# Performance work log

Hardware: AMD Instinct MI355X
Metric: run time of the kernel (lower is better)

## Reference

```python
import jax, jax.numpy as jnp
import numpy as np

EPS = 1e-8  # torch CosineSimilarity default eps

B, T, D, K = 16, 1024, 2048, 64


def setup_inputs() -> dict:
    key = jax.random.key(0)
    k1, k2, k3 = jax.random.split(key, 3)
    inputs = jax.random.normal(k1, (B, T, D), dtype=jnp.float32)
    class_avgs = jax.random.normal(k2, (K, D), dtype=jnp.float32)
    labels = jax.random.randint(k3, (B, T), 0, K, dtype=jnp.int64)
    return {"inputs": inputs, "class_avgs": class_avgs, "labels": labels}


def _simrel_forward(inputs, class_avgs, labels):
    # inputs: [B, T, D]; class_avgs: [K, D]; labels: [B, T] int
    # Faithful training-mode forward: sequential running-mean prototype
    # update per token (row-major over batch then sequence), cosine sims
    # computed against the prototype state *before* each token's update.
    b, t, d = inputs.shape
    k = class_avgs.shape[0]
    vecs = inputs.reshape(b * t, d)
    labs = labels.reshape(b * t)
    class_ids = jnp.arange(k)

    def step(carry, xs):
        avgs, counts = carry          # [K, D], [K]
        vec, label = xs               # [D], scalar int
        nv = jnp.maximum(jnp.sqrt(jnp.sum(vec * vec)), EPS)
        na = jnp.maximum(jnp.sqrt(jnp.sum(avgs * avgs, axis=1)), EPS)  # [K]
        cos = (avgs @ vec) / (na * nv)                                 # [K]
        is_inf = jnp.any(jnp.isinf(avgs), axis=1)                      # [K]
        self_sim = jnp.sum(vec * vec) / (nv * nv)  # cosine(vec, vec)
        is_label = class_ids == label
        sims = jnp.where(is_inf, jnp.where(is_label, self_sim, -1.0), cos)
        # running-mean update of the labeled class prototype
        c = counts[label]
        old = avgs[label]
        new_row = jnp.where(is_inf[label], vec, (old * c + vec) / (c + 1.0))
        avgs = avgs.at[label].set(new_row)
        counts = counts.at[label].add(1.0)
        return (avgs, counts), sims

    counts0 = jnp.zeros((k,), dtype=inputs.dtype)
    (_, _), sims = jax.lax.scan(step, (class_avgs, counts0), (vecs, labs))
    return sims.reshape(b, t, k)


def reference(inputs, class_avgs, labels):
    return _simrel_forward(inputs, class_avgs, labels)
```

## Files before the change

### kernel.cpp

```cpp
#include <hip/hip_runtime.h>
#include <hip/hip_bf16.h>

#define N_TOK 16384
#define DIM 2048
#define KCLS 64
#define JRANGES 32
#define RANGE 512
#define KC 64
#define EPS 1e-8f

typedef short bf16x8 __attribute__((ext_vector_type(8)));
typedef unsigned short u16x8 __attribute__((ext_vector_type(8)));
typedef float f32x4 __attribute__((ext_vector_type(4)));

__device__ __forceinline__ unsigned short f2bf(float f) {
    unsigned u = __float_as_uint(f);
    u += 0x7fffu + ((u >> 16) & 1u);
    return (unsigned short)(u >> 16);
}
__device__ __forceinline__ float bf2f(unsigned short s) {
    return __uint_as_float(((unsigned)s) << 16);
}

__device__ __forceinline__ float dpp_sum64(float x) {
    x += __int_as_float(__builtin_amdgcn_update_dpp(0, __float_as_int(x), 0x111, 0xf, 0xf, true));
    x += __int_as_float(__builtin_amdgcn_update_dpp(0, __float_as_int(x), 0x112, 0xf, 0xf, true));
    x += __int_as_float(__builtin_amdgcn_update_dpp(0, __float_as_int(x), 0x114, 0xf, 0xf, true));
    x += __int_as_float(__builtin_amdgcn_update_dpp(0, __float_as_int(x), 0x118, 0xf, 0xf, true));
    x += __int_as_float(__builtin_amdgcn_update_dpp(0, __float_as_int(x), 0x142, 0xf, 0xf, true));
    x += __int_as_float(__builtin_amdgcn_update_dpp(0, __float_as_int(x), 0x143, 0xf, 0xf, true));
    return x;
}

__global__ __launch_bounds__(256) void prep_kernel(
    const float* __restrict__ x, unsigned short* __restrict__ xb,
    float* __restrict__ vnorm2, const int* __restrict__ raw,
    int* __restrict__ lab, float* __restrict__ n2snap) {
    int bid = blockIdx.x, tid = threadIdx.x;
    if (bid < 64) {
        __shared__ int not64;
        if (tid == 0) not64 = 0;
        __syncthreads();
        int n0 = bid * 256 + tid;
        int lo = raw[2 * n0], hi = raw[2 * n0 + 1];
        if (hi != 0 || lo < 0 || lo >= KCLS) atomicOr(&not64, 1);
        __syncthreads();
        lab[n0] = not64 ? raw[n0] : raw[2 * n0];
    } else if (bid < 72) {
        n2snap[(bid - 64) * 256 + tid] = 0.f;
    }
    int w4 = tid >> 6, lane = tid & 63;
    int n = bid * 4 + w4;
    const float* v = x + (size_t)n * DIM;
    unsigned short* o = xb + (size_t)n * DIM;
    float p = 0.f;
#pragma unroll
    for (int it = 0; it < 8; it++) {
        float4 a = *(const float4*)(v + it * 256 + lane * 4);
        p = fmaf(a.x, a.x, p); p = fmaf(a.y, a.y, p);
        p = fmaf(a.z, a.z, p); p = fmaf(a.w, a.w, p);
        ushort4 h = make_ushort4(f2bf(a.x), f2bf(a.y), f2bf(a.z), f2bf(a.w));
        *(ushort4*)(o + it * 256 + lane * 4) = h;
    }
    p = dpp_sum64(p);
    if (lane == 63) vnorm2[n] = p;
}

__global__ __launch_bounds__(256) void partials_kernel(
    const unsigned short* __restrict__ xb, const int* __restrict__ lab,
    float* __restrict__ spart, int* __restrict__ cnt_range) {
    int bid = blockIdx.x;
    int j = bid & 31, k = bid >> 5;
    int t = threadIdx.x;
    __shared__ int ll[RANGE];
    __shared__ short ml[RANGE];
    __shared__ int nm_s;
    for (int i = t; i < RANGE; i += 256) ll[i] = lab[j * RANGE + i];
    __syncthreads();
    if (t == 0) {
        int nm = 0;
        for (int i = 0; i < RANGE; i++)
            if (ll[i] == k) ml[nm++] = (short)i;
        nm_s = nm;
        cnt_range[j * KCLS + k] = nm;
    }
    __syncthreads();
    int nm = nm_s;
    float acc[8] = {0, 0, 0, 0, 0, 0, 0, 0};
    for (int m = 0; m < nm; m++) {
        const unsigned short* r = xb + (size_t)(j * RANGE + (int)ml[m]) * DIM + t * 8;
        u16x8 hv = *(const u16x8*)r;
#pragma unroll
        for (int i = 0; i < 8; i++) acc[i] += bf2f(hv[i]);
    }
    float* dst = spart + ((size_t)j * KCLS + k) * DIM + t * 8;
    *(float4*)dst = make_float4(acc[0], acc[1], acc[2], acc[3]);
    *(float4*)(dst + 4) = make_float4(acc[4], acc[5], acc[6], acc[7]);
}

__global__ __launch_bounds__(256) void scan_kernel(
    const float* __restrict__ avgs, float* __restrict__ spart,
    unsigned short* __restrict__ Sb, float* __restrict__ n2snap,
    const int* __restrict__ cnt_range, int* __restrict__ cnt_before) {
    int t = blockIdx.x * 256 + threadIdx.x;
    int lane = threadIdx.x & 63;
    int k = t >> 9;
    int d4 = t & 511;
    int d = d4 * 4;
    float4 run = {0, 0, 0, 0};
    int cb = 0;
    float4 init = *(const float4*)(avgs + (size_t)k * DIM + d);
    for (int j = 0; j < JRANGES; j++) {
        size_t idx = ((size_t)j * KCLS + k) * DIM + d;
        float4 part = *(const float4*)(spart + idx);
        float4 w = (cb == 0) ? init : run;
        *(float4*)(spart + idx) = w;
        *(ushort4*)(Sb + idx) = make_ushort4(f2bf(w.x), f2bf(w.y), f2bf(w.z), f2bf(w.w));
        float s = 0.f;
        s = fmaf(w.x, w.x, s); s = fmaf(w.y, w.y, s);
        s = fmaf(w.z, w.z, s); s = fmaf(w.w, w.w, s);
        s = dpp_sum64(s);
        if (lane == 63) atomicAdd(&n2snap[j * KCLS + k], s);
        if (d4 == 0) cnt_before[j * KCLS + k] = cb;
        run.x += part.x; run.y += part.y; run.z += part.z; run.w += part.w;
        cb += cnt_range[j * KCLS + k];
    }
}

__device__ __forceinline__ void stage_panel(
    const unsigned short* __restrict__ src, short* dst, int nunits,
    int t, int kcoff) {
#pragma unroll
    for (int i = 0; i < 2; i++) {
        int u = t + 512 * i;
        if (u < nunits) {
            int row = u >> 3, gsw = u & 7;
            int g = gsw ^ (row & 7);
            const unsigned short* s = src + (size_t)row * DIM + kcoff + g * 8;
            __builtin_amdgcn_global_load_lds(
                (__attribute__((address_space(1))) void*)s,
                (__attribute__((address_space(3))) void*)(dst + u * 8),
                16, 0, 0);
        }
    }
}

__global__ __launch_bounds__(512, 4) void gemm_kernel(
    const unsigned short* __restrict__ xb, const unsigned short* __restrict__ Sb,
    float* __restrict__ D0, unsigned short* __restrict__ Gbf) {
    __shared__ short PI[2][128 * KC];
    __shared__ short PJ[2][128 * KC];
    static const char TIa[14] = {0,1,1,2,2,2,3,3,3,3, 0,1,2,3};
    static const char TJa[14] = {0,0,1,0,1,2,0,1,2,3, 0,0,0,0};

    int bid = blockIdx.x;
    int j = bid & 31;
    int tt = bid >> 5;
    int I = TIa[tt], J = TJa[tt];
    bool isD = (tt >= 10);
    bool diag = (!isD) && (I == J);
    int start = j * RANGE;
    int t = threadIdx.x, lane = t & 63, w = t >> 6;
    int rw = w & 3, cw = w >> 2;
    int NCF = isD ? 2 : 4;
    int colbase = isD ? cw * 32 : cw * 64;

    f32x4 acc[2][4];
#pragma unroll
    for (int a = 0; a < 2; a++)
#pragma unroll
        for (int b = 0; b < 4; b++) acc[a][b] = (f32x4){0.f, 0.f, 0.f, 0.f};

    const unsigned short* srcI = xb + (size_t)(start + I * 128) * DIM;
    const unsigned short* srcJ = isD ? (Sb + (size_t)(j * KCLS) * DIM)
                                     : (xb + (size_t)(start + J * 128) * DIM);
    int nJu = isD ? 512 : 1024;

    stage_panel(srcI, PI[0], 1024, t, 0);
    if (!diag) stage_panel(srcJ, PJ[0], nJu, t, 0);
    __syncthreads();

    for (int kc = 0; kc < DIM / KC; kc++) {
        int cur = kc & 1;
        if (kc + 1 < DIM / KC) {
            stage_panel(srcI, PI[cur ^ 1], 1024, t, (kc + 1) * KC);
            if (!diag) stage_panel(srcJ, PJ[cur ^ 1], nJu, t, (kc + 1) * KC);
        }
        const short* PA = PI[cur];
        const short* PB = diag ? PI[cur] : PJ[cur];
#pragma unroll
        for (int kk = 0; kk < 2; kk++) {
            int kb = kk * 32 + (lane >> 4) * 8;
            int ra = rw * 32 + (lane & 15);
            bf16x8 a0 = *(const bf16x8*)&PA[ra * KC + (kb ^ ((ra & 7) << 3))];
            int ra1 = ra + 16;
            bf16x8 a1 = *(const bf16x8*)&PA[ra1 * KC + (kb ^ ((ra1 & 7) << 3))];
#pragma unroll
            for (int f = 0; f < 4; f++) {
                if (f < NCF) {
                    int rb = colbase + f * 16 + (lane & 15);
                    bf16x8 bb = *(const bf16x8*)&PB[rb * KC + (kb ^ ((rb & 7) << 3))];
                    acc[0][f] = __builtin_amdgcn_mfma_f32_16x16x32_bf16(a0, bb, acc[0][f], 0, 0, 0);
                    acc[1][f] = __builtin_amdgcn_mfma_f32_16x16x32_bf16(a1, bb, acc[1][f], 0, 0, 0);
                }
            }
        }
        __syncthreads();
    }

    if (!isD) {
        size_t gbase = (size_t)j * (512 * 512);
        short* TT = &PI[0][0];
#pragma unroll
        for (int rf = 0; rf < 2; rf++)
#pragma unroll
            for (int f = 0; f < 4; f++)
#pragma unroll
                for (int r = 0; r < 4; r++) {
                    int lr = rw * 32 + rf * 16 + (lane >> 4) * 4 + r;
                    int lc = colbase + f * 16 + (lane & 15);
                    unsigned short hv = f2bf(acc[rf][f][r]);
                    Gbf[gbase + (size_t)(I * 128 + lr) * 512 + J * 128 + lc] = hv;
                    if (I != J)
                        TT[lc * 128 + (lr ^ ((lc & 15) << 3))] = (short)hv;
                }
        if (I != J) {
            __syncthreads();
#pragma unroll
            for (int i = 0; i < 4; i++) {
                int u = t + 512 * i;
                int tr = u >> 4, tc = u & 15;
                u16x8 v = *(const u16x8*)&TT[tr * 128 + ((tc * 8) ^ ((tr & 15) << 3))];
                *(u16x8*)&Gbf[gbase + (size_t)(J * 128 + tr) * 512 + I * 128 + tc * 8] = v;
            }
        }
    } else {
#pragma unroll
        for (int rf = 0; rf < 2; rf++)
#pragma unroll
            for (int f = 0; f < 2; f++)
#pragma unroll
                for (int r = 0; r < 4; r++) {
                    int grow = start + I * 128 + rw * 32 + rf * 16 + (lane >> 4) * 4 + r;
                    int gcol = colbase + f * 16 + (lane & 15);
                    D0[(size_t)grow * KCLS + gcol] = acc[rf][f][r];
                }
    }
}

__global__ __launch_bounds__(512) void finalize_kernel(
    const int* __restrict__ lab, const float* __restrict__ D0,
    const unsigned short* __restrict__ Gbf, const float* __restrict__ vnorm2,
    const float* __restrict__ n2snap, const int* __restrict__ cnt_before,
    float* __restrict__ out) {
    __shared__ unsigned char lbl[RANGE];
    __shared__ short evl[RANGE];
    __shared__ short evcnt_s[8];
    __shared__ short evoff_s[9];
    __shared__ float corrb[8][RANGE];
    __shared__ float cntb[8][RANGE];
    __shared__ float rdv[RANGE];
    __shared__ float invna[RANGE + 8];
    __shared__ unsigned char vgs[8];

    int bid = blockIdx.x;
    int g = bid >> 5, jr = bid & 31;
    int g8 = g * 8;
    int start = jr * RANGE;
    int t = threadIdx.x, lane = t & 63, w = t >> 6;
    int c = g8 + w;

    lbl[t] = (unsigned char)lab[start + t];
    if (t < 8) vgs[t] = (cnt_before[jr * KCLS + g8 + t] == 0) ? 1 : 0;
    __syncthreads();

    unsigned char myl[8];
    int cntL = 0;
#pragma unroll
    for (int i = 0; i < 8; i++) {
        myl[i] = lbl[lane * 8 + i];
        cntL += (myl[i] == c) ? 1 : 0;
    }
    int pre = cntL;
    for (int s = 1; s < 64; s <<= 1) {
        int v = __shfl_up(pre, s, 64);
        if (lane >= s) pre += v;
    }
    int tot = __shfl(pre, 63, 64);
    if (lane == 63) evcnt_s[w] = (short)tot;
    __syncthreads();
    if (t == 0) {
        int s = 0;
        for (int i = 0; i < 8; i++) { evoff_s[i] = (short)s; s += evcnt_s[i]; }
        evoff_s[8] = (short)s;
    }
    __syncthreads();
    int off = evoff_s[w], m = evcnt_s[w];
    {
        int wr = off + (pre - cntL);
#pragma unroll
        for (int i = 0; i < 8; i++)
            if (myl[i] == c) evl[wr++] = (short)(lane * 8 + i);
    }
    __syncthreads();

    const unsigned short* grb = Gbf + (size_t)jr * 262144;
    int vg = vgs[w];
#pragma unroll 1
    for (int chk = 0; chk < 8; chk++) {
        int tk = chk * 64 + lane;
        float corr = 0.f;
        int cnt = 0;
#pragma unroll 1
        for (int i = 0; i < m; i++) {
            int e = evl[off + i];
            float gv = bf2f(grb[(size_t)e * 512 + tk]);
            bool after = (tk > e);
            corr += after ? gv : 0.f;
            cnt += after ? 1 : 0;
        }
        corrb[w][tk] = corr;
        cntb[w][tk] = (float)cnt;
        if ((int)lbl[tk] == c) {
            float d0v = vg ? 0.f : D0[(size_t)(start + tk) * KCLS + c];
            rdv[off + cnt] = d0v + corr;
        }
    }
    __syncthreads();

    if (t < 8) {
        int o = evoff_s[t], mm = evcnt_s[t];
        int vgt = vgs[t];
        float n2 = n2snap[jr * KCLS + g8 + t];
        invna[o + t] = 1.0f / fmaxf(sqrtf(n2), EPS);
        for (int i = 1; i <= mm; i++) {
            int e = evl[o + i - 1];
            float xn2 = vnorm2[start + e];
            if (vgt && i == 1) n2 = xn2;
            else n2 += 2.f * rdv[o + i - 1] + xn2;
            invna[o + t + i] = 1.0f / fmaxf(sqrtf(n2), EPS);
        }
    }
    __syncthreads();

    {
        float4 d0a = *(const float4*)&D0[(size_t)(start + t) * KCLS + g8];
        float4 d0b = *(const float4*)&D0[(size_t)(start + t) * KCLS + g8 + 4];
        float d0[8] = {d0a.x, d0a.y, d0a.z, d0a.w, d0b.x, d0b.y, d0b.z, d0b.w};
        float nvinv = 1.0f / fmaxf(sqrtf(vnorm2[start + t]), EPS);
        float o8[8];
#pragma unroll
        for (int cc = 0; cc < 8; cc++) {
            float corr = corrb[cc][t];
            int cnt = (int)cntb[cc][t];
            float dot = (vgs[cc] && cnt > 0) ? corr : (d0[cc] + corr);
            o8[cc] = dot * invna[evoff_s[cc] + cc + cnt] * nvinv;
        }
        float4 oa = {o8[0], o8[1], o8[2], o8[3]};
        float4 ob = {o8[4], o8[5], o8[6], o8[7]};
        float* op = &out[(size_t)(start + t) * KCLS + g8];
        *(float4*)op = oa;
        *(float4*)(op + 4) = ob;
    }
}

extern "C" void kernel_launch(void* const* d_in, const int* in_sizes, int n_in,
                              void* d_out, int out_size, void* d_ws, size_t ws_size,
                              hipStream_t stream) {
    const float* inputs = (const float*)d_in[0];
    const float* class_avgs = (const float*)d_in[1];
    const int* labels_raw = (const int*)d_in[2];
    float* out = (float*)d_out;
    char* ws = (char*)d_ws;

    size_t off = 0;
    int* lab = (int*)(ws + off);          off += (size_t)N_TOK * 4;
    int* cnt_range = (int*)(ws + off);    off += (size_t)JRANGES * KCLS * 4;
    int* cnt_before = (int*)(ws + off);   off += (size_t)JRANGES * KCLS * 4;
    float* n2snap = (float*)(ws + off);   off += (size_t)JRANGES * KCLS * 4;
    float* vnorm2 = (float*)(ws + off);   off += (size_t)N_TOK * 4;
    off = (off + 255) & ~(size_t)255;
    unsigned short* Xb = (unsigned short*)(ws + off);
    off += (size_t)N_TOK * DIM * 2;
    unsigned short* Sb = (unsigned short*)(ws + off);
    off += (size_t)JRANGES * KCLS * DIM * 2;
    float* D0 = (float*)(ws + off);       off += (size_t)N_TOK * KCLS * 4;
    float* spart = (float*)(ws + off);
    unsigned short* Gbf = (unsigned short*)spart;

    prep_kernel<<<N_TOK / 4, 256, 0, stream>>>(inputs, Xb, vnorm2, labels_raw,
                                               lab, n2snap);
    partials_kernel<<<JRANGES * KCLS, 256, 0, stream>>>(Xb, lab, spart, cnt_range);
    scan_kernel<<<(KCLS * (DIM / 4)) / 256, 256, 0, stream>>>(class_avgs, spart, Sb,
                                                              n2snap, cnt_range,
                                                              cnt_before);
    gemm_kernel<<<14 * JRANGES, 512, 0, stream>>>(Xb, Sb, D0, Gbf);
    finalize_kernel<<<8 * JRANGES, 512, 0, stream>>>(lab, D0, Gbf, vnorm2, n2snap,
                                                     cnt_before, out);
}
```

Baseline: 179.5 us.

## Fuse per-range class partial sums and prefix scan into one per-class kernel

```diff
diff --git a/kernel.cpp b/kernel.cpp
--- a/kernel.cpp
+++ b/kernel.cpp
@@ -35,7 +35,7 @@
 __global__ __launch_bounds__(256) void prep_kernel(
     const float* __restrict__ x, unsigned short* __restrict__ xb,
     float* __restrict__ vnorm2, const int* __restrict__ raw,
-    int* __restrict__ lab, float* __restrict__ n2snap) {
+    int* __restrict__ lab) {
     int bid = blockIdx.x, tid = threadIdx.x;
     if (bid < 64) {
         __shared__ int not64;
@@ -46,8 +46,6 @@
         if (hi != 0 || lo < 0 || lo >= KCLS) atomicOr(&not64, 1);
         __syncthreads();
         lab[n0] = not64 ? raw[n0] : raw[2 * n0];
-    } else if (bid < 72) {
-        n2snap[(bid - 64) * 256 + tid] = 0.f;
     }
     int w4 = tid >> 6, lane = tid & 63;
     int n = bid * 4 + w4;
@@ -66,65 +64,71 @@
     if (lane == 63) vnorm2[n] = p;
 }
 
-__global__ __launch_bounds__(256) void partials_kernel(
+__global__ __launch_bounds__(512) void classscan_kernel(
     const unsigned short* __restrict__ xb, const int* __restrict__ lab,
-    float* __restrict__ spart, int* __restrict__ cnt_range) {
-    int bid = blockIdx.x;
-    int j = bid & 31, k = bid >> 5;
-    int t = threadIdx.x;
-    __shared__ int ll[RANGE];
-    __shared__ short ml[RANGE];
-    __shared__ int nm_s;
-    for (int i = t; i < RANGE; i += 256) ll[i] = lab[j * RANGE + i];
-    __syncthreads();
-    if (t == 0) {
-        int nm = 0;
-        for (int i = 0; i < RANGE; i++)
-            if (ll[i] == k) ml[nm++] = (short)i;
-        nm_s = nm;
-        cnt_range[j * KCLS + k] = nm;
-    }
-    __syncthreads();
-    int nm = nm_s;
-    float acc[8] = {0, 0, 0, 0, 0, 0, 0, 0};
-    for (int m = 0; m < nm; m++) {
-        const unsigned short* r = xb + (size_t)(j * RANGE + (int)ml[m]) * DIM + t * 8;
-        u16x8 hv = *(const u16x8*)r;
-#pragma unroll
-        for (int i = 0; i < 8; i++) acc[i] += bf2f(hv[i]);
-    }
-    float* dst = spart + ((size_t)j * KCLS + k) * DIM + t * 8;
-    *(float4*)dst = make_float4(acc[0], acc[1], acc[2], acc[3]);
-    *(float4*)(dst + 4) = make_float4(acc[4], acc[5], acc[6], acc[7]);
-}
-
-__global__ __launch_bounds__(256) void scan_kernel(
-    const float* __restrict__ avgs, float* __restrict__ spart,
-    unsigned short* __restrict__ Sb, float* __restrict__ n2snap,
-    const int* __restrict__ cnt_range, int* __restrict__ cnt_before) {
-    int t = blockIdx.x * 256 + threadIdx.x;
-    int lane = threadIdx.x & 63;
-    int k = t >> 9;
-    int d4 = t & 511;
-    int d = d4 * 4;
-    float4 run = {0, 0, 0, 0};
-    int cb = 0;
-    float4 init = *(const float4*)(avgs + (size_t)k * DIM + d);
+    const float* __restrict__ avgs, unsigned short* __restrict__ Sb,
+    float* __restrict__ n2snap, int* __restrict__ cnt_before) {
+    __shared__ unsigned char lbl[N_TOK];
+    __shared__ short list[N_TOK];
+    __shared__ int wtot[8];
+    __shared__ float n2loc[JRANGES];
+
+    int k = blockIdx.x;
+    int t = threadIdx.x, lane = t & 63, w = t >> 6;
+
+    for (int i = t; i < N_TOK; i += 512) lbl[i] = (unsigned char)lab[i];
+    if (t < JRANGES) n2loc[t] = 0.f;
+    __syncthreads();
+
+    int base = t * 32;
+    int cnt = 0;
+#pragma unroll
+    for (int i = 0; i < 32; i++) cnt += (lbl[base + i] == k) ? 1 : 0;
+    int pre = cnt;
+    for (int s = 1; s < 64; s <<= 1) {
+        int v = __shfl_up(pre, s, 64);
+        if (lane >= s) pre += v;
+    }
+    if (lane == 63) wtot[w] = pre;
+    __syncthreads();
+    int woff = 0;
+    for (int i = 0; i < w; i++) woff += wtot[i];
+    int total = 0;
+    for (int i = 0; i < 8; i++) total += wtot[i];
+    {
+        int wr = woff + pre - cnt;
+#pragma unroll
+        for (int i = 0; i < 32; i++)
+            if (lbl[base + i] == k) list[wr++] = (short)(base + i);
+    }
+    __syncthreads();
+
+    float4 init = *(const float4*)(avgs + (size_t)k * DIM + t * 4);
+    float4 pref = {0.f, 0.f, 0.f, 0.f};
+    int i = 0;
+#pragma unroll 1
     for (int j = 0; j < JRANGES; j++) {
-        size_t idx = ((size_t)j * KCLS + k) * DIM + d;
-        float4 part = *(const float4*)(spart + idx);
-        float4 w = (cb == 0) ? init : run;
-        *(float4*)(spart + idx) = w;
-        *(ushort4*)(Sb + idx) = make_ushort4(f2bf(w.x), f2bf(w.y), f2bf(w.z), f2bf(w.w));
+        float4 snap = (i == 0) ? init : pref;
+        size_t idx = ((size_t)j * KCLS + k) * DIM + t * 4;
+        *(ushort4*)(Sb + idx) =
+            make_ushort4(f2bf(snap.x), f2bf(snap.y), f2bf(snap.z), f2bf(snap.w));
         float s = 0.f;
-        s = fmaf(w.x, w.x, s); s = fmaf(w.y, w.y, s);
-        s = fmaf(w.z, w.z, s); s = fmaf(w.w, w.w, s);
+        s = fmaf(snap.x, snap.x, s); s = fmaf(snap.y, snap.y, s);
+        s = fmaf(snap.z, snap.z, s); s = fmaf(snap.w, snap.w, s);
         s = dpp_sum64(s);
-        if (lane == 63) atomicAdd(&n2snap[j * KCLS + k], s);
-        if (d4 == 0) cnt_before[j * KCLS + k] = cb;
-        run.x += part.x; run.y += part.y; run.z += part.z; run.w += part.w;
-        cb += cnt_range[j * KCLS + k];
-    }
+        if (lane == 63) atomicAdd(&n2loc[j], s);
+        if (t == 0) cnt_before[j * KCLS + k] = i;
+        int end = (j + 1) * RANGE;
+        while (i < total && (int)list[i] < end) {
+            const unsigned short* r = xb + (size_t)list[i] * DIM + t * 4;
+            ushort4 hv = *(const ushort4*)r;
+            pref.x += bf2f(hv.x); pref.y += bf2f(hv.y);
+            pref.z += bf2f(hv.z); pref.w += bf2f(hv.w);
+            i++;
+        }
+    }
+    __syncthreads();
+    if (t < JRANGES) n2snap[t * KCLS + k] = n2loc[t];
 }
 
 __device__ __forceinline__ void stage_panel(
@@ -375,7 +379,6 @@
 
     size_t off = 0;
     int* lab = (int*)(ws + off);          off += (size_t)N_TOK * 4;
-    int* cnt_range = (int*)(ws + off);    off += (size_t)JRANGES * KCLS * 4;
     int* cnt_before = (int*)(ws + off);   off += (size_t)JRANGES * KCLS * 4;
     float* n2snap = (float*)(ws + off);   off += (size_t)JRANGES * KCLS * 4;
     float* vnorm2 = (float*)(ws + off);   off += (size_t)N_TOK * 4;
@@ -385,15 +388,12 @@
     unsigned short* Sb = (unsigned short*)(ws + off);
     off += (size_t)JRANGES * KCLS * DIM * 2;
     float* D0 = (float*)(ws + off);       off += (size_t)N_TOK * KCLS * 4;
-    float* spart = (float*)(ws + off);
-    unsigned short* Gbf = (unsigned short*)spart;
-
-    prep_kernel<<<N_TOK / 4, 256, 0, stream>>>(inputs, Xb, vnorm2, labels_raw,
-                                               lab, n2snap);
-    partials_kernel<<<JRANGES * KCLS, 256, 0, stream>>>(Xb, lab, spart, cnt_range);
-    scan_kernel<<<(KCLS * (DIM / 4)) / 256, 256, 0, stream>>>(class_avgs, spart, Sb,
-                                                              n2snap, cnt_range,
-                                                              cnt_before);
+    unsigned short* Gbf = (unsigned short*)(ws + off);
+    off += (size_t)JRANGES * 512 * 512 * 2;
+
+    prep_kernel<<<N_TOK / 4, 256, 0, stream>>>(inputs, Xb, vnorm2, labels_raw, lab);
+    classscan_kernel<<<KCLS, 512, 0, stream>>>(Xb, lab, class_avgs, Sb,
+                                               n2snap, cnt_before);
     gemm_kernel<<<14 * JRANGES, 512, 0, stream>>>(Xb, Sb, D0, Gbf);
     finalize_kernel<<<8 * JRANGES, 512, 0, stream>>>(lab, D0, Gbf, vnorm2, n2snap,
                                                      cnt_before, out);
```

After: 228.8 us. +27.4%, slower.
